# Performance work log

Measured on AMD Instinct MI355X. Metric: run time of the kernel, lower is better.

The kernel has to match this reference:

```python
import jax, jax.numpy as jnp
import numpy as np

B, T, D, H = 4, 2048, 1024, 16
HD = D // H  # head_dim = 64


def setup_inputs() -> dict:
    key = jax.random.key(0)
    ks = jax.random.split(key, 7)
    x = jax.random.normal(ks[0], (B, T, D), dtype=jnp.float32)
    engagement = jax.random.uniform(ks[1], (B, T), dtype=jnp.float32)
    mask = jax.random.uniform(ks[2], (B, T)) < 0.1  # True = masked-out key
    s = 1.0 / np.sqrt(D)
    qkv_w = jax.random.normal(ks[3], (3 * D, D), dtype=jnp.float32) * s
    qkv_b = jax.random.normal(ks[4], (3 * D,), dtype=jnp.float32) * 0.02
    out_w = jax.random.normal(ks[5], (D, D), dtype=jnp.float32) * s
    out_b = jax.random.normal(ks[6], (D,), dtype=jnp.float32) * 0.02
    return {"x": x, "engagement": engagement, "mask": mask,
            "qkv_w": qkv_w, "qkv_b": qkv_b, "out_w": out_w, "out_b": out_b}


def reference(x, engagement, mask, qkv_w, qkv_b, out_w, out_b):
    b, t, d = x.shape
    qkv = x @ qkv_w.T + qkv_b                       # [B,T,3D]
    q, k, v = jnp.split(qkv, 3, axis=-1)
    # [B,T,D] -> [B,H,T,HD]
    to_heads = lambda a: a.reshape(b, t, H, HD).transpose(0, 2, 1, 3)
    q, k, v = to_heads(q), to_heads(k), to_heads(v)
    attn = jnp.einsum('bhqd,bhkd->bhqk', q, k) / jnp.sqrt(jnp.float32(HD))
    log_g = jnp.log(jnp.clip(engagement, 1e-6))     # [B,T] per-key bias
    attn = attn + log_g[:, None, None, :]
    attn = jnp.where(mask[:, None, None, :], jnp.float32(-1e9), attn)
    p = jax.nn.softmax(attn, axis=-1)
    o = jnp.einsum('bhqk,bhkd->bhqd', p, v)         # [B,H,T,HD]
    o = o.transpose(0, 2, 1, 3).reshape(b, t, d)    # [B,T,D]
    return o @ out_w.T + out_b
```

## Files before the change

### kernel.cpp

```cpp
#include <hip/hip_runtime.h>
#include <math.h>

#define B_  4
#define T_  2048
#define D_  1024
#define H_  16
#define HD_ 64

typedef unsigned short ushort_t;
typedef unsigned int uint_t;
typedef __attribute__((ext_vector_type(8))) short bf16x8;
typedef __attribute__((ext_vector_type(4))) float f32x4;

#define SC_LOG2 0.1803368801111243f

__device__ inline ushort_t f2bf(float f) {
  uint_t u = __float_as_uint(f);
  u += 0x7fffu + ((u >> 16) & 1u);
  return (ushort_t)(u >> 16);
}
__device__ inline ushort_t f2bf_fast(float f) {
  return (ushort_t)((__float_as_uint(f) + 0x8000u) >> 16);
}
__device__ inline uint_t cvtpk_bf16(float lo, float hi) {
  uint_t r;
  asm("v_cvt_pk_bf16_f32 %0, %1, %2" : "=v"(r) : "v"(lo), "v"(hi));
  return r;
}

__device__ inline void gload_lds16(const ushort_t* g, ushort_t* l) {
  __builtin_amdgcn_global_load_lds(
      (const __attribute__((address_space(1))) unsigned int*)g,
      (__attribute__((address_space(3))) unsigned int*)l, 16, 0, 0);
}

__global__ __launch_bounds__(256) void cvt_bf16(const float* __restrict__ in,
                                                ushort_t* __restrict__ out, int n) {
  int i = (blockIdx.x * 256 + threadIdx.x) * 4;
  if (i + 3 < n) {
    float4 v = *(const float4*)(in + i);
    uint_t lo = (uint_t)f2bf(v.x) | ((uint_t)f2bf(v.y) << 16);
    uint_t hi = (uint_t)f2bf(v.z) | ((uint_t)f2bf(v.w) << 16);
    *(uint2*)(out + i) = make_uint2(lo, hi);
  }
}

__global__ __launch_bounds__(256) void bias_prep(const float* __restrict__ eng,
                                                 const int* __restrict__ mask,
                                                 float* __restrict__ biasA, int n) {
  int i = blockIdx.x * 256 + threadIdx.x;
  if (i < n) biasA[i] = mask[i] ? -1e30f : __log2f(fmaxf(eng[i], 1e-6f));
}

#define CHUNKS_ 32

#define STAGE_CHUNK(CK, SLOT)                                                  \
  {                                                                            \
    const int ck_ = (CK);                                                      \
    ushort_t* sb_ = lds + (SLOT) * 12288;                                      \
    gload_lds16(Ag + (size_t)ck_ * 32, sb_ + w * 512);                         \
    gload_lds16(Bg + (size_t)ck_ * 32, sb_ + 4096 + w * 1024);                 \
    gload_lds16(Bg + 16384 + (size_t)ck_ * 32, sb_ + 4096 + w * 1024 + 512);   \
  }

template <int WRITE_BF16>
__global__ __launch_bounds__(512, 4) void gemm256(
    const ushort_t* __restrict__ A, const ushort_t* __restrict__ Bm,
    const float* __restrict__ bias, void* __restrict__ Cout,
    int N, int nbx) {
  __shared__ __align__(16) ushort_t lds[36864];

  const int tid = threadIdx.x;
  const int w = tid >> 6, lane = tid & 63;
  const int l15 = lane & 15, quad = lane >> 4;
  const int wr = w >> 2, wc = w & 3;

  int wg = blockIdx.x;
  const int cpx = gridDim.x >> 3;
  wg = (wg & 7) * cpx + (wg >> 3);
  const int m0 = (wg / nbx) * 128, n0 = (wg % nbx) * 256;

  const int gc = (lane & 3) ^ ((lane >> 3) & 3);
  const ushort_t* Ag = A + (size_t)(m0 + w * 16 + (lane >> 2)) * 1024 + gc * 8;
  const ushort_t* Bg = Bm + (size_t)(n0 + w * 32 + (lane >> 2)) * 1024 + gc * 8;

  const int p8 = (quad ^ ((l15 >> 1) & 3)) * 8;
  const int rowA = (wr * 64 + l15) * 32 + p8;
  const int rowB = 4096 + (wc * 64 + l15) * 32 + p8;

  f32x4 acc[4][4];
#pragma unroll
  for (int mb = 0; mb < 4; ++mb)
#pragma unroll
    for (int nb = 0; nb < 4; ++nb) acc[mb][nb] = (f32x4){0.f, 0.f, 0.f, 0.f};

  STAGE_CHUNK(0, 0);
  STAGE_CHUNK(1, 1);
  asm volatile("s_waitcnt vmcnt(3)" ::: "memory");
  __builtin_amdgcn_s_barrier();
  __builtin_amdgcn_sched_barrier(0);

  int s_cur = 0;
#pragma unroll 1
  for (int ph = 0; ph < CHUNKS_; ++ph) {
    const ushort_t* Ls = lds + s_cur * 12288;
    bf16x8 af[4], bf[4];
#pragma unroll
    for (int mb = 0; mb < 4; ++mb)
      af[mb] = *(const bf16x8*)(Ls + rowA + mb * 512);
#pragma unroll
    for (int nb = 0; nb < 4; ++nb)
      bf[nb] = *(const bf16x8*)(Ls + rowB + nb * 512);
    if (ph < CHUNKS_ - 2) {
      const int s_n2 = (s_cur == 0) ? 2 : s_cur - 1;
      STAGE_CHUNK(ph + 2, s_n2);
    }
    __builtin_amdgcn_s_setprio(1);
#pragma unroll
    for (int mb = 0; mb < 4; ++mb)
#pragma unroll
      for (int nb = 0; nb < 4; ++nb)
        acc[mb][nb] = __builtin_amdgcn_mfma_f32_16x16x32_bf16(
            af[mb], bf[nb], acc[mb][nb], 0, 0, 0);
    __builtin_amdgcn_s_setprio(0);
    if (ph < CHUNKS_ - 2)
      asm volatile("s_waitcnt vmcnt(3)" ::: "memory");
    else
      asm volatile("s_waitcnt vmcnt(0)" ::: "memory");
    __builtin_amdgcn_s_barrier();
    __builtin_amdgcn_sched_barrier(0);
    s_cur = (s_cur == 2) ? 0 : s_cur + 1;
  }

  float bb[4];
#pragma unroll
  for (int nb = 0; nb < 4; ++nb) bb[nb] = bias[n0 + wc * 64 + nb * 16 + l15];

  if (WRITE_BF16) {
    ushort_t* patch = lds + w * 4608;
    ushort_t* Cb = (ushort_t*)Cout;
#pragma unroll
    for (int mb = 0; mb < 4; ++mb)
#pragma unroll
      for (int nb = 0; nb < 4; ++nb)
#pragma unroll
        for (int i = 0; i < 4; ++i)
          patch[(mb * 16 + quad * 4 + i) * 72 + nb * 16 + l15] =
              f2bf_fast(acc[mb][nb][i] + bb[nb]);
#pragma unroll
    for (int it = 0; it < 8; ++it) {
      int rl = it * 8 + (lane >> 3);
      size_t grow = (size_t)(m0 + wr * 64 + rl);
      uint4 v = *(const uint4*)&patch[rl * 72 + (lane & 7) * 8];
      *(uint4*)&Cb[grow * N + n0 + wc * 64 + (lane & 7) * 8] = v;
    }
  } else {
    float* Cf = (float*)Cout;
#pragma unroll
    for (int mb = 0; mb < 4; ++mb)
#pragma unroll
      for (int i = 0; i < 4; ++i) {
        size_t row = (size_t)(m0 + wr * 64 + mb * 16 + quad * 4 + i);
#pragma unroll
        for (int nb = 0; nb < 4; ++nb)
          Cf[row * N + n0 + wc * 64 + nb * 16 + l15] = acc[mb][nb][i] + bb[nb];
      }
  }
}

#define ATTN_TILE(K0, Kc, Vc, bc, Kn, Vn, bn, PF)                              \
  {                                                                            \
    uint4 va_, vc_;                                                            \
    const bool pf_ = (PF);                                                     \
    if (pf_) {                                                                 \
      const int k1_ = (K0) + 64;                                               \
      _Pragma("unroll")                                                        \
      for (int u = 0; u < 2; ++u)                                              \
        gload_lds16(kbase + (size_t)(k1_ + w * 16 + u * 8 + kr) * rs + kgc * 8,\
                    &(Kn)[(w * 16 + u * 8) * 64]);                             \
      const ushort_t* vp_ = vbase + (size_t)(k1_ + 2 * kp) * rs + cc * 8;      \
      va_ = *(const uint4*)vp_;                                                \
      vc_ = *(const uint4*)(vp_ + rs);                                         \
      if (tid < 64) (bn)[tid] = bptr[k1_ + tid];                               \
    }                                                                          \
    bf16x8 kf0[4], kf1[4];                                                     \
    _Pragma("unroll")                                                          \
    for (int nb = 0; nb < 4; ++nb) {                                           \
      int key = nb * 16 + l15;                                                 \
      int p0 = (quad ^ (key & 7)) * 8;                                         \
      kf0[nb] = *(const bf16x8*)(&(Kc)[key * 64 + p0]);                        \
      kf1[nb] = *(const bf16x8*)(&(Kc)[key * 64 + (p0 ^ 32)]);                 \
    }                                                                          \
    bf16x8 vf0[4], vf1[4];                                                     \
    _Pragma("unroll")                                                          \
    for (int nbd = 0; nbd < 4; ++nbd) {                                        \
      vf0[nbd] = *(const bf16x8*)(&(Vc)[quad * 520 + (nbd * 16 + l15) * 8]);   \
      vf1[nbd] =                                                               \
          *(const bf16x8*)(&(Vc)[(4 + quad) * 520 + (nbd * 16 + l15) * 8]);    \
    }                                                                          \
    _Pragma("unroll")                                                          \
    for (int qb = 0; qb < 2; ++qb) {                                           \
      f32x4 st[4];                                                             \
      __builtin_amdgcn_s_setprio(1);                                           \
      _Pragma("unroll")                                                        \
      for (int nb = 0; nb < 4; ++nb) {                                         \
        f32x4 s = (f32x4){0.f, 0.f, 0.f, 0.f};                                 \
        s = __builtin_amdgcn_mfma_f32_16x16x32_bf16(kf0[nb], qf[qb][0], s, 0,  \
                                                    0, 0);                     \
        s = __builtin_amdgcn_mfma_f32_16x16x32_bf16(kf1[nb], qf[qb][1], s, 0,  \
                                                    0, 0);                     \
        st[nb] = s;                                                            \
      }                                                                        \
      __builtin_amdgcn_s_setprio(0);                                           \
      float pp[4][4];                                                          \
      float racc = 0.f;                                                        \
      _Pragma("unroll")                                                        \
      for (int nb = 0; nb < 4; ++nb) {                                         \
        f32x4 bv = *(const f32x4*)&(bc)[nb * 16 + quad * 4];                   \
        _Pragma("unroll")                                                      \
        for (int i = 0; i < 4; ++i) {                                          \
          float p = __builtin_amdgcn_exp2f(st[nb][i] * SC_LOG2 + bv[i]);       \
          pp[nb][i] = p;                                                       \
          racc += p;                                                           \
        }                                                                      \
      }                                                                        \
      rsum[qb] += racc;                                                        \
      union { uint4 u; bf16x8 v; } pf0, pf1;                                   \
      pf0.u.x = cvtpk_bf16(pp[0][0], pp[0][1]);                                \
      pf0.u.y = cvtpk_bf16(pp[0][2], pp[0][3]);                                \
      pf0.u.z = cvtpk_bf16(pp[1][0], pp[1][1]);                                \
      pf0.u.w = cvtpk_bf16(pp[1][2], pp[1][3]);                                \
      pf1.u.x = cvtpk_bf16(pp[2][0], pp[2][1]);                                \
      pf1.u.y = cvtpk_bf16(pp[2][2], pp[2][3]);                                \
      pf1.u.z = cvtpk_bf16(pp[3][0], pp[3][1]);                                \
      pf1.u.w = cvtpk_bf16(pp[3][2], pp[3][3]);                                \
      __builtin_amdgcn_s_setprio(1);                                           \
      _Pragma("unroll")                                                        \
      for (int nbd = 0; nbd < 4; ++nbd) {                                      \
        Oa[qb][nbd] = __builtin_amdgcn_mfma_f32_16x16x32_bf16(                 \
            pf0.v, vf0[nbd], Oa[qb][nbd], 0, 0, 0);                            \
        Oa[qb][nbd] = __builtin_amdgcn_mfma_f32_16x16x32_bf16(                 \
            pf1.v, vf1[nbd], Oa[qb][nbd], 0, 0, 0);                            \
      }                                                                        \
      __builtin_amdgcn_s_setprio(0);                                           \
    }                                                                          \
    if (pf_) {                                                                 \
      uint_t* dst_ = (uint_t*)&(Vn)[gp * 520 + cc * 64 + j0];                  \
      dst_[0]  = (va_.x & 0xffffu) | (vc_.x << 16);                            \
      dst_[4]  = (va_.x >> 16)     | (vc_.x & 0xffff0000u);                    \
      dst_[8]  = (va_.y & 0xffffu) | (vc_.y << 16);                            \
      dst_[12] = (va_.y >> 16)     | (vc_.y & 0xffff0000u);                    \
      dst_[16] = (va_.z & 0xffffu) | (vc_.z << 16);                            \
      dst_[20] = (va_.z >> 16)     | (vc_.z & 0xffff0000u);                    \
      dst_[24] = (va_.w & 0xffffu) | (vc_.w << 16);                            \
      dst_[28] = (va_.w >> 16)     | (vc_.w & 0xffff0000u);                    \
    }                                                                          \
    __syncthreads();                                                           \
  }

__global__ __launch_bounds__(256) void attn_mfma(
    const ushort_t* __restrict__ qkv, const float* __restrict__ biasA,
    ushort_t* __restrict__ oat) {
  __shared__ __align__(16) char smem[34048];
  ushort_t* Kb0 = (ushort_t*)(smem);
  ushort_t* Kb1 = (ushort_t*)(smem + 8192);
  ushort_t* Vb0 = (ushort_t*)(smem + 16384);
  ushort_t* Vb1 = (ushort_t*)(smem + 24704);
  float* bsh0 = (float*)(smem + 33024);
  float* bsh1 = (float*)(smem + 33280);
  float (*lsum)[32] = (float (*)[32])(smem + 33536);

  const int b = blockIdx.z, h = blockIdx.y;
  const int q0 = blockIdx.x * 128;
  const int tid = threadIdx.x;
  const int w = tid >> 6, lane = tid & 63;
  const int l15 = lane & 15, quad = lane >> 4;
  const size_t rs = 3 * D_;

  bf16x8 qf[2][2];
#pragma unroll
  for (int qb = 0; qb < 2; ++qb) {
    const ushort_t* qp =
        qkv + (size_t)(b * T_ + q0 + w * 32 + qb * 16 + l15) * rs + h * HD_;
    qf[qb][0] = *(const bf16x8*)(qp + quad * 8);
    qf[qb][1] = *(const bf16x8*)(qp + 32 + quad * 8);
  }

  f32x4 Oa[2][4];
#pragma unroll
  for (int qb = 0; qb < 2; ++qb)
#pragma unroll
    for (int nb = 0; nb < 4; ++nb) Oa[qb][nb] = (f32x4){0.f, 0.f, 0.f, 0.f};
  float rsum[2] = {0.f, 0.f};

  const ushort_t* kbase = qkv + (size_t)(b * T_) * rs + D_ + h * HD_;
  const ushort_t* vbase = kbase + D_;
  const float* bptr = biasA + b * T_;

  const int kr = lane >> 3, kc = lane & 7;
  const int kgc = kc ^ kr;
  const int kp = tid & 31, cc = tid >> 5;
  const int gp = (kp >> 4) * 4 + ((kp >> 1) & 3);
  const int j0 = ((kp >> 3) & 1) * 4 + 2 * (kp & 1);

  {
#pragma unroll
    for (int u = 0; u < 2; ++u)
      gload_lds16(kbase + (size_t)(w * 16 + u * 8 + kr) * rs + kgc * 8,
                  &Kb0[(w * 16 + u * 8) * 64]);
    const ushort_t* vp = vbase + (size_t)(2 * kp) * rs + cc * 8;
    uint4 va = *(const uint4*)vp;
    uint4 vc = *(const uint4*)(vp + rs);
    if (tid < 64) bsh0[tid] = bptr[tid];
    uint_t* dst = (uint_t*)&Vb0[gp * 520 + cc * 64 + j0];
    dst[0]  = (va.x & 0xffffu) | (vc.x << 16);
    dst[4]  = (va.x >> 16)     | (vc.x & 0xffff0000u);
    dst[8]  = (va.y & 0xffffu) | (vc.y << 16);
    dst[12] = (va.y >> 16)     | (vc.y & 0xffff0000u);
    dst[16] = (va.z & 0xffffu) | (vc.z << 16);
    dst[20] = (va.z >> 16)     | (vc.z & 0xffff0000u);
    dst[24] = (va.w & 0xffffu) | (vc.w << 16);
    dst[28] = (va.w >> 16)     | (vc.w & 0xffff0000u);
  }
  __syncthreads();

  for (int k0 = 0; k0 < T_; k0 += 128) {
    ATTN_TILE(k0,      Kb0, Vb0, bsh0, Kb1, Vb1, bsh1, true);
    ATTN_TILE(k0 + 64, Kb1, Vb1, bsh1, Kb0, Vb0, bsh0, k0 + 128 < T_);
  }

#pragma unroll
  for (int qb = 0; qb < 2; ++qb) {
    float r = rsum[qb];
    r += __shfl_xor(r, 16, 64);
    r += __shfl_xor(r, 32, 64);
    if (lane < 16) lsum[w][qb * 16 + lane] = r;
  }
  ushort_t* OstW = (ushort_t*)(smem) + w * (32 * 72);
#pragma unroll
  for (int qb = 0; qb < 2; ++qb) {
    f32x4 lr = *(const f32x4*)&lsum[w][qb * 16 + quad * 4];
    f32x4 invl;
#pragma unroll
    for (int i = 0; i < 4; ++i) invl[i] = __builtin_amdgcn_rcpf(lr[i]);
#pragma unroll
    for (int nbd = 0; nbd < 4; ++nbd)
#pragma unroll
      for (int i = 0; i < 4; ++i)
        OstW[(qb * 16 + quad * 4 + i) * 72 + nbd * 16 + l15] =
            f2bf_fast(Oa[qb][nbd][i] * invl[i]);
  }
  ushort_t* dst = oat + (size_t)(b * T_ + q0 + w * 32) * D_ + h * HD_;
#pragma unroll
  for (int pp = 0; pp < 4; ++pp) {
    int row = pp * 8 + (lane >> 3), c = lane & 7;
    uint4 v = *(const uint4*)&OstW[row * 72 + c * 8];
    *(uint4*)&dst[(size_t)row * D_ + c * 8] = v;
  }
}

extern "C" void kernel_launch(void* const* d_in, const int* in_sizes, int n_in,
                              void* d_out, int out_size, void* d_ws, size_t ws_size,
                              hipStream_t stream) {
  const float* x     = (const float*)d_in[0];
  const float* eng   = (const float*)d_in[1];
  const int*   mask  = (const int*)d_in[2];
  const float* qkv_w = (const float*)d_in[3];
  const float* qkv_b = (const float*)d_in[4];
  const float* out_w = (const float*)d_in[5];
  const float* out_b = (const float*)d_in[6];
  float* out = (float*)d_out;

  const int M = B_ * T_;
  const size_t nx = (size_t)M * D_;
  const size_t nwq = (size_t)3 * D_ * D_;
  const size_t nwo = (size_t)D_ * D_;
  const size_t nqkv = (size_t)M * 3 * D_;

  char* p = (char*)d_ws;
  ushort_t* xb    = (ushort_t*)p;            p += nx * 2;
  ushort_t* wqkvb = (ushort_t*)p;            p += nwq * 2;
  ushort_t* woutb = (ushort_t*)p;            p += nwo * 2;
  ushort_t* qkvb  = (ushort_t*)p;            p += nqkv * 2;
  ushort_t* oatb  = (ushort_t*)p;            p += nx * 2;
  float*    biasA = (float*)p;               p += (size_t)M * 4;

  cvt_bf16<<<(int)(nx / 1024), 256, 0, stream>>>(x, xb, (int)nx);
  cvt_bf16<<<(int)(nwq / 1024), 256, 0, stream>>>(qkv_w, wqkvb, (int)nwq);
  cvt_bf16<<<(int)(nwo / 1024), 256, 0, stream>>>(out_w, woutb, (int)nwo);
  bias_prep<<<M / 256, 256, 0, stream>>>(eng, mask, biasA, M);

  gemm256<1><<<768, 512, 0, stream>>>(xb, wqkvb, qkv_b, qkvb, 3 * D_, 12);
  attn_mfma<<<dim3(T_ / 128, H_, B_), 256, 0, stream>>>(qkvb, biasA, oatb);
  gemm256<0><<<256, 512, 0, stream>>>(oatb, woutb, out_b, out, D_, 4);
}
```

Baseline: 295.9 us.

## Double attention query tile per block and narrow output-projection GEMM tile

The attention kernel now uses 512 threads and 256 queries per block. Each K/V tile staged in shared memory is therefore reused by twice as many waves. The K load is redistributed across 8 waves, and only half the threads do the V transpose loads. The output projection GEMM is templated to use a 128-wide N tile, which doubles its grid to 512 blocks for better CU occupancy, at the cost of less reuse of each A tile.

```diff
diff --git a/kernel.cpp b/kernel.cpp
--- a/kernel.cpp
+++ b/kernel.cpp
@@ -57,18 +57,25 @@
 #define STAGE_CHUNK(CK, SLOT)                                                  \
   {                                                                            \
     const int ck_ = (CK);                                                      \
-    ushort_t* sb_ = lds + (SLOT) * 12288;                                      \
+    ushort_t* sb_ = lds + (SLOT) * SLOT_E;                                     \
     gload_lds16(Ag + (size_t)ck_ * 32, sb_ + w * 512);                         \
-    gload_lds16(Bg + (size_t)ck_ * 32, sb_ + 4096 + w * 1024);                 \
-    gload_lds16(Bg + 16384 + (size_t)ck_ * 32, sb_ + 4096 + w * 1024 + 512);   \
-  }
-
-template <int WRITE_BF16>
+    if constexpr (BN == 256) {                                                 \
+      gload_lds16(Bg + (size_t)ck_ * 32, sb_ + 4096 + w * 1024);               \
+      gload_lds16(Bg + 16384 + (size_t)ck_ * 32, sb_ + 4096 + w * 1024 + 512); \
+    } else {                                                                   \
+      gload_lds16(Bg + (size_t)ck_ * 32, sb_ + 4096 + w * 512);                \
+    }                                                                          \
+  }
+
+template <int WRITE_BF16, int BN>
 __global__ __launch_bounds__(512, 4) void gemm256(
     const ushort_t* __restrict__ A, const ushort_t* __restrict__ Bm,
     const float* __restrict__ bias, void* __restrict__ Cout,
     int N, int nbx) {
-  __shared__ __align__(16) ushort_t lds[36864];
+  constexpr int SLOT_E = 4096 + BN * 32;
+  constexpr int NBB = BN / 64;
+  constexpr int WCOLS = BN / 4;
+  __shared__ __align__(16) ushort_t lds[3 * SLOT_E];
 
   const int tid = threadIdx.x;
   const int w = tid >> 6, lane = tid & 63;
@@ -78,38 +85,42 @@
   int wg = blockIdx.x;
   const int cpx = gridDim.x >> 3;
   wg = (wg & 7) * cpx + (wg >> 3);
-  const int m0 = (wg / nbx) * 128, n0 = (wg % nbx) * 256;
+  const int m0 = (wg / nbx) * 128, n0 = (wg % nbx) * BN;
 
   const int gc = (lane & 3) ^ ((lane >> 3) & 3);
   const ushort_t* Ag = A + (size_t)(m0 + w * 16 + (lane >> 2)) * 1024 + gc * 8;
-  const ushort_t* Bg = Bm + (size_t)(n0 + w * 32 + (lane >> 2)) * 1024 + gc * 8;
+  const ushort_t* Bg =
+      Bm + (size_t)(n0 + w * (BN / 8) + (lane >> 2)) * 1024 + gc * 8;
 
   const int p8 = (quad ^ ((l15 >> 1) & 3)) * 8;
   const int rowA = (wr * 64 + l15) * 32 + p8;
-  const int rowB = 4096 + (wc * 64 + l15) * 32 + p8;
-
-  f32x4 acc[4][4];
+  const int rowB = 4096 + (wc * WCOLS + l15) * 32 + p8;
+
+  f32x4 acc[4][NBB];
 #pragma unroll
   for (int mb = 0; mb < 4; ++mb)
 #pragma unroll
-    for (int nb = 0; nb < 4; ++nb) acc[mb][nb] = (f32x4){0.f, 0.f, 0.f, 0.f};
+    for (int nb = 0; nb < NBB; ++nb) acc[mb][nb] = (f32x4){0.f, 0.f, 0.f, 0.f};
 
   STAGE_CHUNK(0, 0);
   STAGE_CHUNK(1, 1);
-  asm volatile("s_waitcnt vmcnt(3)" ::: "memory");
+  if constexpr (BN == 256)
+    asm volatile("s_waitcnt vmcnt(3)" ::: "memory");
+  else
+    asm volatile("s_waitcnt vmcnt(2)" ::: "memory");
   __builtin_amdgcn_s_barrier();
   __builtin_amdgcn_sched_barrier(0);
 
   int s_cur = 0;
 #pragma unroll 1
   for (int ph = 0; ph < CHUNKS_; ++ph) {
-    const ushort_t* Ls = lds + s_cur * 12288;
-    bf16x8 af[4], bf[4];
+    const ushort_t* Ls = lds + s_cur * SLOT_E;
+    bf16x8 af[4], bf[NBB];
 #pragma unroll
     for (int mb = 0; mb < 4; ++mb)
       af[mb] = *(const bf16x8*)(Ls + rowA + mb * 512);
 #pragma unroll
-    for (int nb = 0; nb < 4; ++nb)
+    for (int nb = 0; nb < NBB; ++nb)
       bf[nb] = *(const bf16x8*)(Ls + rowB + nb * 512);
     if (ph < CHUNKS_ - 2) {
       const int s_n2 = (s_cur == 0) ? 2 : s_cur - 1;
@@ -119,30 +130,35 @@
 #pragma unroll
     for (int mb = 0; mb < 4; ++mb)
 #pragma unroll
-      for (int nb = 0; nb < 4; ++nb)
+      for (int nb = 0; nb < NBB; ++nb)
         acc[mb][nb] = __builtin_amdgcn_mfma_f32_16x16x32_bf16(
             af[mb], bf[nb], acc[mb][nb], 0, 0, 0);
     __builtin_amdgcn_s_setprio(0);
-    if (ph < CHUNKS_ - 2)
-      asm volatile("s_waitcnt vmcnt(3)" ::: "memory");
-    else
+    if (ph < CHUNKS_ - 2) {
+      if constexpr (BN == 256)
+        asm volatile("s_waitcnt vmcnt(3)" ::: "memory");
+      else
+        asm volatile("s_waitcnt vmcnt(2)" ::: "memory");
+    } else {
       asm volatile("s_waitcnt vmcnt(0)" ::: "memory");
+    }
     __builtin_amdgcn_s_barrier();
     __builtin_amdgcn_sched_barrier(0);
     s_cur = (s_cur == 2) ? 0 : s_cur + 1;
   }
 
-  float bb[4];
-#pragma unroll
-  for (int nb = 0; nb < 4; ++nb) bb[nb] = bias[n0 + wc * 64 + nb * 16 + l15];
-
-  if (WRITE_BF16) {
+  float bb[NBB];
+#pragma unroll
+  for (int nb = 0; nb < NBB; ++nb)
+    bb[nb] = bias[n0 + wc * WCOLS + nb * 16 + l15];
+
+  if constexpr (WRITE_BF16) {
     ushort_t* patch = lds + w * 4608;
     ushort_t* Cb = (ushort_t*)Cout;
 #pragma unroll
     for (int mb = 0; mb < 4; ++mb)
 #pragma unroll
-      for (int nb = 0; nb < 4; ++nb)
+      for (int nb = 0; nb < NBB; ++nb)
 #pragma unroll
         for (int i = 0; i < 4; ++i)
           patch[(mb * 16 + quad * 4 + i) * 72 + nb * 16 + l15] =
@@ -152,7 +168,7 @@
       int rl = it * 8 + (lane >> 3);
       size_t grow = (size_t)(m0 + wr * 64 + rl);
       uint4 v = *(const uint4*)&patch[rl * 72 + (lane & 7) * 8];
-      *(uint4*)&Cb[grow * N + n0 + wc * 64 + (lane & 7) * 8] = v;
+      *(uint4*)&Cb[grow * N + n0 + wc * WCOLS + (lane & 7) * 8] = v;
     }
   } else {
     float* Cf = (float*)Cout;
@@ -162,8 +178,9 @@
       for (int i = 0; i < 4; ++i) {
         size_t row = (size_t)(m0 + wr * 64 + mb * 16 + quad * 4 + i);
 #pragma unroll
-        for (int nb = 0; nb < 4; ++nb)
-          Cf[row * N + n0 + wc * 64 + nb * 16 + l15] = acc[mb][nb][i] + bb[nb];
+        for (int nb = 0; nb < NBB; ++nb)
+          Cf[row * N + n0 + wc * WCOLS + nb * 16 + l15] =
+              acc[mb][nb][i] + bb[nb];
       }
   }
 }
@@ -174,13 +191,13 @@
     const bool pf_ = (PF);                                                     \
     if (pf_) {                                                                 \
       const int k1_ = (K0) + 64;                                               \
-      _Pragma("unroll")                                                        \
-      for (int u = 0; u < 2; ++u)                                              \
-        gload_lds16(kbase + (size_t)(k1_ + w * 16 + u * 8 + kr) * rs + kgc * 8,\
-                    &(Kn)[(w * 16 + u * 8) * 64]);                             \
-      const ushort_t* vp_ = vbase + (size_t)(k1_ + 2 * kp) * rs + cc * 8;      \
-      va_ = *(const uint4*)vp_;                                                \
-      vc_ = *(const uint4*)(vp_ + rs);                                         \
+      gload_lds16(kbase + (size_t)(k1_ + w * 8 + kr8) * rs + kgc * 8,          \
+                  &(Kn)[(w * 8) * 64]);                                        \
+      if (tid < 256) {                                                         \
+        const ushort_t* vp_ = vbase + (size_t)(k1_ + 2 * kp) * rs + cc * 8;    \
+        va_ = *(const uint4*)vp_;                                              \
+        vc_ = *(const uint4*)(vp_ + rs);                                       \
+      }                                                                        \
       if (tid < 64) (bn)[tid] = bptr[k1_ + tid];                               \
     }                                                                          \
     bf16x8 kf0[4], kf1[4];                                                     \
@@ -244,7 +261,7 @@
       }                                                                        \
       __builtin_amdgcn_s_setprio(0);                                           \
     }                                                                          \
-    if (pf_) {                                                                 \
+    if (pf_ && tid < 256) {                                                    \
       uint_t* dst_ = (uint_t*)&(Vn)[gp * 520 + cc * 64 + j0];                  \
       dst_[0]  = (va_.x & 0xffffu) | (vc_.x << 16);                            \
       dst_[4]  = (va_.x >> 16)     | (vc_.x & 0xffff0000u);                    \
@@ -258,20 +275,20 @@
     __syncthreads();                                                           \
   }
 
-__global__ __launch_bounds__(256) void attn_mfma(
+__global__ __launch_bounds__(512) void attn_mfma(
     const ushort_t* __restrict__ qkv, const float* __restrict__ biasA,
     ushort_t* __restrict__ oat) {
-  __shared__ __align__(16) char smem[34048];
+  __shared__ __align__(16) char smem[37888];
   ushort_t* Kb0 = (ushort_t*)(smem);
   ushort_t* Kb1 = (ushort_t*)(smem + 8192);
   ushort_t* Vb0 = (ushort_t*)(smem + 16384);
   ushort_t* Vb1 = (ushort_t*)(smem + 24704);
   float* bsh0 = (float*)(smem + 33024);
   float* bsh1 = (float*)(smem + 33280);
-  float (*lsum)[32] = (float (*)[32])(smem + 33536);
+  float (*lsum)[32] = (float (*)[32])(smem + 36864);
 
   const int b = blockIdx.z, h = blockIdx.y;
-  const int q0 = blockIdx.x * 128;
+  const int q0 = blockIdx.x * 256;
   const int tid = threadIdx.x;
   const int w = tid >> 6, lane = tid & 63;
   const int l15 = lane & 15, quad = lane >> 4;
@@ -297,30 +314,30 @@
   const ushort_t* vbase = kbase + D_;
   const float* bptr = biasA + b * T_;
 
-  const int kr = lane >> 3, kc = lane & 7;
-  const int kgc = kc ^ kr;
+  const int kr8 = lane >> 3;
+  const int kgc = (lane & 7) ^ kr8;
   const int kp = tid & 31, cc = tid >> 5;
   const int gp = (kp >> 4) * 4 + ((kp >> 1) & 3);
   const int j0 = ((kp >> 3) & 1) * 4 + 2 * (kp & 1);
 
   {
-#pragma unroll
-    for (int u = 0; u < 2; ++u)
-      gload_lds16(kbase + (size_t)(w * 16 + u * 8 + kr) * rs + kgc * 8,
-                  &Kb0[(w * 16 + u * 8) * 64]);
-    const ushort_t* vp = vbase + (size_t)(2 * kp) * rs + cc * 8;
-    uint4 va = *(const uint4*)vp;
-    uint4 vc = *(const uint4*)(vp + rs);
+    gload_lds16(kbase + (size_t)(w * 8 + kr8) * rs + kgc * 8,
+                &Kb0[(w * 8) * 64]);
+    if (tid < 256) {
+      const ushort_t* vp = vbase + (size_t)(2 * kp) * rs + cc * 8;
+      uint4 va = *(const uint4*)vp;
+      uint4 vc = *(const uint4*)(vp + rs);
+      uint_t* dst = (uint_t*)&Vb0[gp * 520 + cc * 64 + j0];
+      dst[0]  = (va.x & 0xffffu) | (vc.x << 16);
+      dst[4]  = (va.x >> 16)     | (vc.x & 0xffff0000u);
+      dst[8]  = (va.y & 0xffffu) | (vc.y << 16);
+      dst[12] = (va.y >> 16)     | (vc.y & 0xffff0000u);
+      dst[16] = (va.z & 0xffffu) | (vc.z << 16);
+      dst[20] = (va.z >> 16)     | (vc.z & 0xffff0000u);
+      dst[24] = (va.w & 0xffffu) | (vc.w << 16);
+      dst[28] = (va.w >> 16)     | (vc.w & 0xffff0000u);
+    }
     if (tid < 64) bsh0[tid] = bptr[tid];
-    uint_t* dst = (uint_t*)&Vb0[gp * 520 + cc * 64 + j0];
-    dst[0]  = (va.x & 0xffffu) | (vc.x << 16);
-    dst[4]  = (va.x >> 16)     | (vc.x & 0xffff0000u);
-    dst[8]  = (va.y & 0xffffu) | (vc.y << 16);
-    dst[12] = (va.y >> 16)     | (vc.y & 0xffff0000u);
-    dst[16] = (va.z & 0xffffu) | (vc.z << 16);
-    dst[20] = (va.z >> 16)     | (vc.z & 0xffff0000u);
-    dst[24] = (va.w & 0xffffu) | (vc.w << 16);
-    dst[28] = (va.w >> 16)     | (vc.w & 0xffff0000u);
   }
   __syncthreads();
 
@@ -336,7 +353,7 @@
     r += __shfl_xor(r, 32, 64);
     if (lane < 16) lsum[w][qb * 16 + lane] = r;
   }
-  ushort_t* OstW = (ushort_t*)(smem) + w * (32 * 72);
+  ushort_t* OstW = (ushort_t*)(smem) + w * 2304;
 #pragma unroll
   for (int qb = 0; qb < 2; ++qb) {
     f32x4 lr = *(const f32x4*)&lsum[w][qb * 16 + quad * 4];
@@ -390,7 +407,7 @@
   cvt_bf16<<<(int)(nwo / 1024), 256, 0, stream>>>(out_w, woutb, (int)nwo);
   bias_prep<<<M / 256, 256, 0, stream>>>(eng, mask, biasA, M);
 
-  gemm256<1><<<768, 512, 0, stream>>>(xb, wqkvb, qkv_b, qkvb, 3 * D_, 12);
-  attn_mfma<<<dim3(T_ / 128, H_, B_), 256, 0, stream>>>(qkvb, biasA, oatb);
-  gemm256<0><<<256, 512, 0, stream>>>(oatb, woutb, out_b, out, D_, 4);
-}
+  gemm256<1, 256><<<768, 512, 0, stream>>>(xb, wqkvb, qkv_b, qkvb, 3 * D_, 12);
+  attn_mfma<<<dim3(T_ / 256, H_, B_), 512, 0, stream>>>(qkvb, biasA, oatb);
+  gemm256<0, 128><<<512, 512, 0, stream>>>(oatb, woutb, out_b, out, D_, 8);
+}
```

Result: faster. 282.6 us (-4.5%).
